# Kernel tuning notes

Measured on AMD Instinct MI355X. Metric: run time of the kernel, lower is better.

Reference implementation:

```python
import jax, jax.numpy as jnp
import numpy as np

EMBED_DIM = 16
GAMMA0 = 1.0
GAMMA = 1.0
ZETA = 1.0
INV_T = 1.0
EPS = 1e-8


def setup_inputs() -> dict:
    key = jax.random.key(0)
    z = jax.random.normal(key, (16, 131072, EMBED_DIM), dtype=jnp.float32)
    return {"z": z}


def _entropy(p):
    # H = -sum p log(p + 1e-8) over last axis
    return -(p * jnp.log(p + EPS)).sum(-1)


def reference(z):
    # L2 normalize over embed dim (torch F.normalize clamps norm at 1e-12)
    norm = jnp.linalg.norm(z, axis=-1, keepdims=True)
    z = z / jnp.maximum(norm, 1e-12)

    # soft entropy loss
    p = jax.nn.sigmoid(-4.0 * z / (EMBED_DIM ** 0.5 * INV_T))  # (..., g)
    prob = jnp.stack([p, 1.0 - p], axis=-1)                     # (..., g, 2)
    persample_entropy = _entropy(prob).sum(-1).mean()           # scalar
    avg_prob = prob.reshape(-1, EMBED_DIM, 2).mean(0)           # (g, 2)
    cb_entropy = _entropy(avg_prob).sum()                       # scalar
    entropy_penalty = GAMMA0 * persample_entropy - GAMMA * cb_entropy

    # sign quantize with straight-through estimator
    zhat = jnp.where(z > 0, 1.0, -1.0).astype(z.dtype)
    zq = z + jax.lax.stop_gradient(zhat - z)

    # bit-pack codes -> indices (fits int32 for embed_dim=16)
    basis = (2 ** jnp.arange(EMBED_DIM - 1, -1, -1, dtype=jnp.int32))
    bits = ((jax.lax.stop_gradient(zq) + 1.0) * 0.5).astype(jnp.int32)
    indices = (bits * basis).sum(-1)

    zq = zq * (1.0 / EMBED_DIM ** 0.5)
    loss = ZETA * entropy_penalty / INV_T
    return zq, loss, indices, avg_prob
```

## Files before the change

kernel.cpp:

```cpp
#include <hip/hip_runtime.h>
#include <math.h>


__global__ __launch_bounds__(256) void bsq_main(
    const float* __restrict__ z,
    float* __restrict__ zq,
    float* __restrict__ idx_out,
    float* __restrict__ ws_h,
    float* __restrict__ ws_p,
    long long quads)
{
    const int tid = threadIdx.x;
    const long long stride = (long long)gridDim.x * blockDim.x;
    long long q = (long long)blockIdx.x * blockDim.x + tid;

    const int c = tid & 3;

    float h_acc = 0.f;
    float p_acc[4] = {0.f, 0.f, 0.f, 0.f};

    for (; q < quads; q += stride) {
        const float4 v = reinterpret_cast<const float4*>(z)[q];
        float vv[4] = {v.x, v.y, v.z, v.w};

        float ss = v.x*v.x + v.y*v.y + v.z*v.z + v.w*v.w;
        ss += __shfl_xor(ss, 1);
        ss += __shfl_xor(ss, 2);
        const float scale = rsqrtf(fmaxf(ss, 1e-24f));

        unsigned bits = 0u;
        float4 o;
        float* op = &o.x;
        #pragma unroll
        for (int j = 0; j < 4; ++j) {
            const float s   = vv[j] * scale;
            const float e   = __expf(s);
            const float inv = 1.0f / (1.0f + e);
            const float h   = __logf(1.0f + e) - s * (1.0f - inv);
            h_acc    += h;
            p_acc[j] += inv;
            const bool bit = vv[j] > 0.0f;
            op[j] = bit ? 0.25f : -0.25f;
            bits |= (bit ? 1u : 0u) << (15 - (4 * c + j));
        }
        reinterpret_cast<float4*>(zq)[q] = o;

        bits |= __shfl_xor(bits, 1);
        bits |= __shfl_xor(bits, 2);
        if (c == 0) idx_out[q >> 2] = (float)bits;
    }

    #pragma unroll
    for (int m = 32; m >= 4; m >>= 1) {
        h_acc += __shfl_xor(h_acc, m);
        #pragma unroll
        for (int j = 0; j < 4; ++j) p_acc[j] += __shfl_xor(p_acc[j], m);
    }
    h_acc += __shfl_xor(h_acc, 2);
    h_acc += __shfl_xor(h_acc, 1);

    __shared__ float sh_h[4];
    __shared__ float sh_p[4][16];
    const int wave = tid >> 6;
    const int lane = tid & 63;
    if (lane == 0) sh_h[wave] = h_acc;
    if (lane < 4) {
        #pragma unroll
        for (int j = 0; j < 4; ++j) sh_p[wave][4 * lane + j] = p_acc[j];
    }
    __syncthreads();

    if (tid == 0)
        ws_h[blockIdx.x] = sh_h[0] + sh_h[1] + sh_h[2] + sh_h[3];
    if (tid < 16)
        ws_p[(long long)tid * gridDim.x + blockIdx.x] =
            sh_p[0][tid] + sh_p[1][tid] + sh_p[2][tid] + sh_p[3][tid];
}

__global__ __launch_bounds__(1024) void bsq_final(
    const float* __restrict__ ws_h,
    const float* __restrict__ ws_p,
    float* __restrict__ loss_out,
    float* __restrict__ avgp_out,
    int nb, long long rows)
{
    const int tid  = threadIdx.x;
    const int wave = tid >> 6;
    const int lane = tid & 63;
    const double invR = 1.0 / (double)rows;

    __shared__ double sh_q[16];
    __shared__ double sh_h;

    double p = 0.0;
    for (int i = lane; i < nb; i += 64)
        p += (double)ws_p[(long long)wave * nb + i];

    double h = 0.0;
    if (wave == 0)
        for (int i = lane; i < nb; i += 64)
            h += (double)ws_h[i];

    #pragma unroll
    for (int m = 32; m >= 1; m >>= 1)
        p += __shfl_xor(p, m);
    if (wave == 0) {
        #pragma unroll
        for (int m = 32; m >= 1; m >>= 1)
            h += __shfl_xor(h, m);
        if (lane == 0) sh_h = h * invR;
    }
    if (lane == 0) sh_q[wave] = p * invR;
    __syncthreads();

    if (wave == 0) {
        const double q = (lane < 16) ? sh_q[lane] : 0.0;
        double term = 0.0;
        if (lane < 16)
            term = -(q * log(q + 1e-8) + (1.0 - q) * log((1.0 - q) + 1e-8));
        #pragma unroll
        for (int m = 32; m >= 1; m >>= 1)
            term += __shfl_xor(term, m);
        if (lane == 0)
            loss_out[0] = (float)(sh_h - term);
        if (lane < 16) {
            avgp_out[2 * lane]     = (float)sh_q[lane];
            avgp_out[2 * lane + 1] = (float)(1.0 - sh_q[lane]);
        }
    }
}

extern "C" void kernel_launch(void* const* d_in, const int* in_sizes, int n_in,
                              void* d_out, int out_size, void* d_ws, size_t ws_size,
                              hipStream_t stream) {
    const float* z = (const float*)d_in[0];
    const long long n    = in_sizes[0];
    const long long rows = n / 16;
    const long long quads = n / 4;

    float* out   = (float*)d_out;
    float* zq    = out;
    float* loss  = out + n;
    float* idx   = out + n + 1;
    float* avgp  = out + n + 1 + rows;

    const int NB = 2048;
    float* ws_h = (float*)d_ws;
    float* ws_p = ws_h + NB;

    bsq_main<<<NB, 256, 0, stream>>>(z, zq, idx, ws_h, ws_p, quads);
    bsq_final<<<1, 1024, 0, stream>>>(ws_h, ws_p, loss, avgp, NB, rows);
}
```

Before: 74.71 us.

## Replace exp/log entropy with Taylor polynomials and process one row per thread

Switches from four threads per row with shuffles to one thread handling a full 16-element row via four float4 loads and stores. The sigmoid and binary entropy are replaced by even-order polynomial expansions in s², valid because |s|≤1 after normalisation, with the constant terms (ln2 per element, 0.5 per probability) added back in the final kernel. This removes the transcendental work and the intra-row shuffles, but it truncates the series, which adds approximation error, and the per-thread strided row access may reduce coalescing.

```diff
diff --git a/kernel.cpp b/kernel.cpp
--- a/kernel.cpp
+++ b/kernel.cpp
@@ -8,65 +8,69 @@
     float* __restrict__ idx_out,
     float* __restrict__ ws_h,
     float* __restrict__ ws_p,
-    long long quads)
+    long long rows)
 {
     const int tid = threadIdx.x;
     const long long stride = (long long)gridDim.x * blockDim.x;
-    long long q = (long long)blockIdx.x * blockDim.x + tid;
 
-    const int c = tid & 3;
+    const float C1 = -0.125f,      C2 = 1.0f/64.0f,  C3 = -1.0f/576.0f, C4 = 119.0f/645120.0f;
+    const float D0 = -0.25f,       D1 = 1.0f/48.0f,  D2 = -1.0f/480.0f, D3 = 17.0f/80640.0f;
 
     float h_acc = 0.f;
-    float p_acc[4] = {0.f, 0.f, 0.f, 0.f};
+    float sg[16];
+    #pragma unroll
+    for (int j = 0; j < 16; ++j) sg[j] = 0.f;
 
-    for (; q < quads; q += stride) {
-        const float4 v = reinterpret_cast<const float4*>(z)[q];
-        float vv[4] = {v.x, v.y, v.z, v.w};
+    for (long long r = (long long)blockIdx.x * blockDim.x + tid; r < rows; r += stride) {
+        const float4* zr = reinterpret_cast<const float4*>(z) + (r << 2);
+        float4 q0 = zr[0], q1 = zr[1], q2 = zr[2], q3 = zr[3];
+        float v[16] = {q0.x,q0.y,q0.z,q0.w, q1.x,q1.y,q1.z,q1.w,
+                       q2.x,q2.y,q2.z,q2.w, q3.x,q3.y,q3.z,q3.w};
 
-        float ss = v.x*v.x + v.y*v.y + v.z*v.z + v.w*v.w;
-        ss += __shfl_xor(ss, 1);
-        ss += __shfl_xor(ss, 2);
+        float ss = 0.f;
+        #pragma unroll
+        for (int j = 0; j < 16; ++j) ss = fmaf(v[j], v[j], ss);
         const float scale = rsqrtf(fmaxf(ss, 1e-24f));
 
         unsigned bits = 0u;
-        float4 o;
-        float* op = &o.x;
+        float o[16];
         #pragma unroll
-        for (int j = 0; j < 4; ++j) {
-            const float s   = vv[j] * scale;
-            const float e   = __expf(s);
-            const float inv = 1.0f / (1.0f + e);
-            const float h   = __logf(1.0f + e) - s * (1.0f - inv);
-            h_acc    += h;
-            p_acc[j] += inv;
-            const bool bit = vv[j] > 0.0f;
-            op[j] = bit ? 0.25f : -0.25f;
-            bits |= (bit ? 1u : 0u) << (15 - (4 * c + j));
+        for (int j = 0; j < 16; ++j) {
+            const float s = v[j] * scale;
+            const float t = s * s;
+            const float gp = fmaf(t, fmaf(t, fmaf(t, D3, D2), D1), D0);
+            sg[j] = fmaf(s, gp, sg[j]);
+            const float hin = fmaf(t, fmaf(t, fmaf(t, C4, C3), C2), C1);
+            h_acc = fmaf(t, hin, h_acc);
+
+            const bool bit = v[j] > 0.0f;
+            o[j] = bit ? 0.25f : -0.25f;
+            bits |= (bit ? 1u : 0u) << (15 - j);
         }
-        reinterpret_cast<float4*>(zq)[q] = o;
 
-        bits |= __shfl_xor(bits, 1);
-        bits |= __shfl_xor(bits, 2);
-        if (c == 0) idx_out[q >> 2] = (float)bits;
+        float4* zo = reinterpret_cast<float4*>(zq) + (r << 2);
+        zo[0] = make_float4(o[0],o[1],o[2],o[3]);
+        zo[1] = make_float4(o[4],o[5],o[6],o[7]);
+        zo[2] = make_float4(o[8],o[9],o[10],o[11]);
+        zo[3] = make_float4(o[12],o[13],o[14],o[15]);
+        idx_out[r] = (float)bits;
     }
 
     #pragma unroll
-    for (int m = 32; m >= 4; m >>= 1) {
+    for (int m = 32; m >= 1; m >>= 1) {
         h_acc += __shfl_xor(h_acc, m);
         #pragma unroll
-        for (int j = 0; j < 4; ++j) p_acc[j] += __shfl_xor(p_acc[j], m);
+        for (int j = 0; j < 16; ++j) sg[j] += __shfl_xor(sg[j], m);
     }
-    h_acc += __shfl_xor(h_acc, 2);
-    h_acc += __shfl_xor(h_acc, 1);
 
     __shared__ float sh_h[4];
     __shared__ float sh_p[4][16];
     const int wave = tid >> 6;
     const int lane = tid & 63;
-    if (lane == 0) sh_h[wave] = h_acc;
-    if (lane < 4) {
+    if (lane == 0) {
+        sh_h[wave] = h_acc;
         #pragma unroll
-        for (int j = 0; j < 4; ++j) sh_p[wave][4 * lane + j] = p_acc[j];
+        for (int j = 0; j < 16; ++j) sh_p[wave][j] = sg[j];
     }
     __syncthreads();
 
@@ -88,6 +92,7 @@
     const int wave = tid >> 6;
     const int lane = tid & 63;
     const double invR = 1.0 / (double)rows;
+    const double LN2 = 0.6931471805599453;
 
     __shared__ double sh_q[16];
     __shared__ double sh_h;
@@ -108,9 +113,9 @@
         #pragma unroll
         for (int m = 32; m >= 1; m >>= 1)
             h += __shfl_xor(h, m);
-        if (lane == 0) sh_h = h * invR;
+        if (lane == 0) sh_h = 16.0 * LN2 + h * invR;
     }
-    if (lane == 0) sh_q[wave] = p * invR;
+    if (lane == 0) sh_q[wave] = 0.5 + p * invR;
     __syncthreads();
 
     if (wave == 0) {
@@ -136,7 +141,6 @@
     const float* z = (const float*)d_in[0];
     const long long n    = in_sizes[0];
     const long long rows = n / 16;
-    const long long quads = n / 4;
 
     float* out   = (float*)d_out;
     float* zq    = out;
@@ -148,6 +152,6 @@
     float* ws_h = (float*)d_ws;
     float* ws_p = ws_h + NB;
 
-    bsq_main<<<NB, 256, 0, stream>>>(z, zq, idx, ws_h, ws_p, quads);
+    bsq_main<<<NB, 256, 0, stream>>>(z, zq, idx, ws_h, ws_p, rows);
     bsq_final<<<1, 1024, 0, stream>>>(ws_h, ws_p, loss, avgp, NB, rows);
 }
```

After: 138.2 us. +85.0%, slower.
